# Kernel optimization log

Measured on AMD Instinct MI355X. Metric: run time of the kernel, lower is better.

## Reference

```python
import jax, jax.numpy as jnp
import numpy as np
from math import sqrt

N_HEADS = 4
IN_FEATURES = 64
KQ = 64
HEAD_V = IN_FEATURES // N_HEADS  # 16


def setup_inputs() -> dict:
    key = jax.random.key(0)
    ks = jax.random.split(key, 7)
    s = 0.05
    x = jax.random.normal(ks[0], (8192, IN_FEATURES), dtype=jnp.float32)
    # Per-head Linear weights stacked on a leading head axis.
    # torch Linear: y = x @ W.T + b; we store W already transposed: [H, F, E]
    Wq = jax.random.normal(ks[1], (N_HEADS, IN_FEATURES, KQ), dtype=jnp.float32) * s
    bq = jax.random.normal(ks[2], (N_HEADS, KQ), dtype=jnp.float32) * s
    Wk = jax.random.normal(ks[3], (N_HEADS, IN_FEATURES, KQ), dtype=jnp.float32) * s
    bk = jax.random.normal(ks[4], (N_HEADS, KQ), dtype=jnp.float32) * s
    Wv = jax.random.normal(ks[5], (N_HEADS, IN_FEATURES, HEAD_V), dtype=jnp.float32) * s
    bv = jax.random.normal(ks[6], (N_HEADS, HEAD_V), dtype=jnp.float32) * s
    return {"x": x, "Wq": Wq, "bq": bq, "Wk": Wk, "bk": bk, "Wv": Wv, "bv": bv}


def reference(x, Wq, bq, Wk, bk, Wv, bv):
    N, F = x.shape
    scale = 1.0 / sqrt(F)  # original divides by sqrt(in_features), NOT sqrt(kq)
    # Batched-head projections: [H, N, E]
    Q = jnp.einsum('nf,hfe->hne', x, Wq) + bq[:, None, :]
    K = jnp.einsum('nf,hfe->hne', x, Wk) + bk[:, None, :]
    V = jnp.einsum('nf,hfd->hnd', x, Wv) + bv[:, None, :]
    logits = jnp.einsum('hne,hme->hnm', Q, K) * scale  # [H, N, N]
    attn = jax.nn.softmax(logits, axis=-1)
    out_heads = jnp.einsum('hnm,hmd->hnd', attn, V)    # [H, N, HEAD_V]
    # Head i writes columns [i*HEAD_V:(i+1)*HEAD_V] of the output.
    out = jnp.transpose(out_heads, (1, 0, 2)).reshape(N, F)
    return out
```

## Files before the change

kernel.cpp:

```cpp
#include <hip/hip_runtime.h>

typedef __attribute__((ext_vector_type(4))) float f32x4;
typedef __attribute__((ext_vector_type(8))) short bf16x8;
typedef __attribute__((ext_vector_type(4))) short bf16x4;
typedef long fp8x8;

#define NH 4

static __device__ __forceinline__ unsigned short f2bf(float f){
  unsigned u = __float_as_uint(f);
  u += 0x7FFFu + ((u >> 16) & 1u);
  return (unsigned short)(u >> 16);
}

static __device__ __forceinline__ unsigned pack2bf(float a, float b){
  return __builtin_amdgcn_perm(__float_as_uint(b) + 0x8000u,
                               __float_as_uint(a) + 0x8000u, 0x07060302u);
}

static __device__ __forceinline__ int pack_fp8x4(float a, float b, float c, float d){
  int w = __builtin_amdgcn_cvt_pk_fp8_f32(a, b, 0, false);
  w     = __builtin_amdgcn_cvt_pk_fp8_f32(c, d, w, true);
  return w;
}

__global__ __launch_bounds__(256) void wprep_kernel(
    const float* __restrict__ Wq, const float* __restrict__ bq,
    const float* __restrict__ Wk, const float* __restrict__ bk,
    const float* __restrict__ Wv,
    unsigned short* __restrict__ WF, float* __restrict__ bias_s, int n)
{
  __shared__ unsigned short wqT[64*72];
  __shared__ unsigned short wkT[64*72];
  __shared__ unsigned short wvT[16*72];

  const int t = threadIdx.x;
  const int h = blockIdx.x;
  const float S1 = 0.4246609001f;
  const int f = t >> 2, eg = t & 3;

  {
    const float4* g = (const float4*)(Wq + h*4096 + f*64 + eg*16);
    #pragma unroll
    for (int p = 0; p < 4; ++p){
      float4 d = g[p];
      int e0 = eg*16 + p*4;
      wqT[(e0+0)*72 + f] = f2bf(d.x * S1);
      wqT[(e0+1)*72 + f] = f2bf(d.y * S1);
      wqT[(e0+2)*72 + f] = f2bf(d.z * S1);
      wqT[(e0+3)*72 + f] = f2bf(d.w * S1);
    }
  }
  {
    const float4* g = (const float4*)(Wk + h*4096 + f*64 + eg*16);
    #pragma unroll
    for (int p = 0; p < 4; ++p){
      float4 d = g[p];
      int e0 = eg*16 + p*4;
      wkT[(e0+0)*72 + f] = f2bf(d.x * S1);
      wkT[(e0+1)*72 + f] = f2bf(d.y * S1);
      wkT[(e0+2)*72 + f] = f2bf(d.z * S1);
      wkT[(e0+3)*72 + f] = f2bf(d.w * S1);
    }
  }
  {
    float4 d = *(const float4*)(Wv + h*1024 + f*16 + eg*4);
    int d0 = eg*4;
    wvT[(d0+0)*72 + f] = f2bf(d.x);
    wvT[(d0+1)*72 + f] = f2bf(d.y);
    wvT[(d0+2)*72 + f] = f2bf(d.z);
    wvT[(d0+3)*72 + f] = f2bf(d.w);
  }
  if (t < 64)       bias_s[h*128 + t] = bq[h*64 + t] * S1;
  else if (t < 128) bias_s[h*128 + t] = bk[h*64 + (t-64)] * S1;
  __syncthreads();

  const int lane = t & 63, w = t >> 6;
  const int quad = lane >> 4, l16 = lane & 15;
  for (int s = w; s < 18; s += 4){
    const unsigned short* src;
    if (s < 8){      int jt = s>>1,     ks = s&1;     src = wqT + (jt*16+l16)*72 + ks*32 + quad*8; }
    else if (s < 16){int ft = (s-8)>>1, ks = (s-8)&1; src = wkT + (ft*16+l16)*72 + ks*32 + quad*8; }
    else {           int ks = s-16;                   src = wvT + l16*72 + ks*32 + quad*8; }
    uint4 v = *(const uint4*)src;
    *(uint4*)(WF + ((size_t)(h*18 + s)*64 + lane)*8) = v;
  }
}

__global__ __launch_bounds__(256) void proj_kernel(
    const float* __restrict__ x, const float* __restrict__ bv,
    const unsigned short* __restrict__ WF, const float* __restrict__ bias_s,
    unsigned char* __restrict__ Qt, unsigned char* __restrict__ Kt,
    unsigned short* __restrict__ Vt, int n)
{
  __shared__ unsigned short xf[8*64*8];
  __shared__ float bql[64], bkl[64], bvl[16];

  const int t  = threadIdx.x;
  const int h  = blockIdx.y;
  const int r0 = blockIdx.x * 64;

  {
    const int r = t >> 2, cg4 = t & 3;
    const float4* g = (const float4*)(x + (size_t)(r0 + r)*64 + cg4*16);
    float4 a = g[0], b = g[1], c = g[2], d = g[3];
    unsigned u0 = pack2bf(a.x,a.y), u1 = pack2bf(a.z,a.w);
    unsigned u2 = pack2bf(b.x,b.y), u3 = pack2bf(b.z,b.w);
    unsigned u4 = pack2bf(c.x,c.y), u5 = pack2bf(c.z,c.w);
    unsigned u6 = pack2bf(d.x,d.y), u7 = pack2bf(d.z,d.w);
    const int it = r >> 4, l16r = r & 15, ks = cg4 >> 1, q0 = (cg4 & 1)*2;
    uint4* dst0 = (uint4*)(xf + ((it*2+ks)*64 + q0*16     + l16r)*8);
    uint4* dst1 = (uint4*)(xf + ((it*2+ks)*64 + (q0+1)*16 + l16r)*8);
    *dst0 = make_uint4(u0,u1,u2,u3);
    *dst1 = make_uint4(u4,u5,u6,u7);
  }
  if (t < 64)        bql[t]     = bias_s[h*128 + t];
  else if (t < 128)  bkl[t-64]  = bias_s[h*128 + t];
  else if (t < 144)  bvl[t-128] = bv[h*16 + (t-128)];
  __syncthreads();

  const int lane = t & 63, w = t >> 6;
  const int quad = lane >> 4, l16 = lane & 15;

  bf16x8 xa[8];
  #pragma unroll
  for (int i = 0; i < 8; ++i)
    xa[i] = *(const bf16x8*)(xf + (i*64 + lane)*8);

  const unsigned short* WFh = WF + (size_t)h*18*64*8;
  bf16x8 wq[8];
  #pragma unroll
  for (int s = 0; s < 8; ++s)
    wq[s] = *(const bf16x8*)(WFh + ((size_t)s*64 + lane)*8);
  bf16x8 wk0 = *(const bf16x8*)(WFh + ((size_t)(8 + w*2 + 0)*64 + lane)*8);
  bf16x8 wk1 = *(const bf16x8*)(WFh + ((size_t)(8 + w*2 + 1)*64 + lane)*8);
  bf16x8 wv0 = *(const bf16x8*)(WFh + ((size_t)16*64 + lane)*8);
  bf16x8 wv1 = *(const bf16x8*)(WFh + ((size_t)17*64 + lane)*8);

  const f32x4 z = {0.f,0.f,0.f,0.f};
  f32x4 accQ[4] = {z,z,z,z};
  f32x4 accK[4] = {z,z,z,z};
  f32x4 accV = z;

  #pragma unroll
  for (int jt = 0; jt < 4; ++jt){
    accQ[jt] = __builtin_amdgcn_mfma_f32_16x16x32_bf16(xa[w*2+0], wq[jt*2+0], accQ[jt], 0,0,0);
    accQ[jt] = __builtin_amdgcn_mfma_f32_16x16x32_bf16(xa[w*2+1], wq[jt*2+1], accQ[jt], 0,0,0);
  }
  #pragma unroll
  for (int tt = 0; tt < 4; ++tt){
    accK[tt] = __builtin_amdgcn_mfma_f32_16x16x32_bf16(wk0, xa[tt*2+0], accK[tt], 0,0,0);
    accK[tt] = __builtin_amdgcn_mfma_f32_16x16x32_bf16(wk1, xa[tt*2+1], accK[tt], 0,0,0);
  }
  accV = __builtin_amdgcn_mfma_f32_16x16x32_bf16(xa[w*2+0], wv0, accV, 0,0,0);
  accV = __builtin_amdgcn_mfma_f32_16x16x32_bf16(xa[w*2+1], wv1, accV, 0,0,0);

  #pragma unroll
  for (int jt = 0; jt < 4; ++jt){
    float bqv = bql[jt*16 + l16];
    unsigned o = pack_fp8x4(accQ[jt][0]+bqv, accQ[jt][1]+bqv,
                            accQ[jt][2]+bqv, accQ[jt][3]+bqv);
    *(unsigned*)(Qt + ((size_t)(h*64 + jt*16 + l16))*n + r0 + w*16 + quad*4) = o;
  }
  {
    const int f0 = w*16 + quad*4;
    const float bk0 = bkl[f0], bk1 = bkl[f0+1], bk2 = bkl[f0+2], bk3 = bkl[f0+3];
    const int qk = (f0 & 31) >> 3, hf = f0 >> 5, boff = (quad & 1) * 4;
    #pragma unroll
    for (int tt = 0; tt < 4; ++tt){
      unsigned o = pack_fp8x4(accK[tt][0]+bk0, accK[tt][1]+bk1,
                              accK[tt][2]+bk2, accK[tt][3]+bk3);
      const int T = (r0 >> 4) + tt;
      *(unsigned*)(Kt + (size_t)h*((size_t)n<<6) + (size_t)T*1024
                      + (qk*16 + l16)*16 + hf*8 + boff) = o;
    }
  }
  {
    float bvv = bvl[l16];
    unsigned v01 = pack2bf(accV[0]+bvv, accV[1]+bvv);
    unsigned v23 = pack2bf(accV[2]+bvv, accV[3]+bvv);
    const int T = (r0 >> 4) + w;
    *(uint2*)(Vt + (size_t)h*((size_t)n<<4) + ((size_t)T*64 + lane)*4) = make_uint2(v01, v23);
  }
}

__global__ __launch_bounds__(512) void attn_kernel(
    const unsigned char* __restrict__ Qt, const unsigned char* __restrict__ Kt,
    const unsigned short* __restrict__ Vt, float* __restrict__ out, int n)
{
  __shared__ float part[6][64][17];

  const int tid  = threadIdx.x;
  const int lane = tid & 63;
  const int w    = tid >> 6;
  const int rg   = w >> 2;
  const int jq   = w & 3;
  const int bid  = blockIdx.x;
  const int h    = bid & 3;
  const int iblk = bid >> 2;
  const int l16  = lane & 15, quad = lane >> 4;
  const int i0   = iblk*64 + rg*32;
  const int ntiles = (n >> 2) >> 4;
  const int tile0  = jq * ntiles;

  const unsigned char* qh = Qt + (size_t)(h*64)*n;
  fp8x8 qf[4];
  #pragma unroll
  for (int v = 0; v < 4; ++v){
    const int row0 = i0 + (v >> 1)*16;
    const int kb   = (v & 1)*32;
    const unsigned char* qp = qh + (size_t)(kb + quad*8)*n + row0 + l16;
    unsigned u0 = 0, u1 = 0;
    #pragma unroll
    for (int j = 0; j < 4; ++j) u0 |= (unsigned)qp[(size_t)j*n] << (8*j);
    #pragma unroll
    for (int j = 0; j < 4; ++j) u1 |= (unsigned)qp[(size_t)(j+4)*n] << (8*j);
    qf[v] = (fp8x8)(((unsigned long long)u1 << 32) | (unsigned long long)u0);
  }
  const fp8x8 qf00 = qf[0], qf01 = qf[1], qf10 = qf[2], qf11 = qf[3];

  const uint4* ktu = (const uint4*)(Kt + (size_t)h*((size_t)n<<6)) + (size_t)tile0*64 + lane;
  const uint2* vtu = (const uint2*)(Vt + (size_t)h*((size_t)n<<4)) + (size_t)tile0*64 + lane;

  f32x4 o0  = {0.f,0.f,0.f,0.f};
  f32x4 o1  = {0.f,0.f,0.f,0.f};
  f32x4 la0 = {0.f,0.f,0.f,0.f};
  f32x4 la1 = {0.f,0.f,0.f,0.f};
  const f32x4 z = {0.f,0.f,0.f,0.f};
  const bf16x4 vones = {(short)0x3F80, (short)0x3F80, (short)0x3F80, (short)0x3F80};

  uint4 ka = ktu[0];
  uint2 va = vtu[0];
  uint4 kb = ktu[64];
  uint2 vb = vtu[64];

  for (int tt = 0; tt < ntiles; tt += 2){
    int tn = tt + 2; if (tn >= ntiles) tn = 0;
    uint4 kc = ktu[(size_t)tn*64];
    uint2 vc = vtu[(size_t)tn*64];
    uint4 kd = ktu[(size_t)(tn+1)*64];
    uint2 vd = vtu[(size_t)(tn+1)*64];

    {
      fp8x8 k0 = (fp8x8)(((unsigned long long)ka.y << 32) | ka.x);
      fp8x8 k1 = (fp8x8)(((unsigned long long)ka.w << 32) | ka.z);
      bf16x4 vf; { union { uint2 u; bf16x4 v; } c; c.u = va; vf = c.v; }

      f32x4 s0 = __builtin_amdgcn_mfma_f32_16x16x32_fp8_fp8(k0, qf00, z, 0, 0, 0);
      s0 = __builtin_amdgcn_mfma_f32_16x16x32_fp8_fp8(k1, qf01, s0, 0, 0, 0);
      f32x4 s1 = __builtin_amdgcn_mfma_f32_16x16x32_fp8_fp8(k0, qf10, z, 0, 0, 0);
      s1 = __builtin_amdgcn_mfma_f32_16x16x32_fp8_fp8(k1, qf11, s1, 0, 0, 0);

      float p00 = __builtin_amdgcn_exp2f(s0[0]);
      float p01 = __builtin_amdgcn_exp2f(s0[1]);
      float p02 = __builtin_amdgcn_exp2f(s0[2]);
      float p03 = __builtin_amdgcn_exp2f(s0[3]);
      float p10 = __builtin_amdgcn_exp2f(s1[0]);
      float p11 = __builtin_amdgcn_exp2f(s1[1]);
      float p12 = __builtin_amdgcn_exp2f(s1[2]);
      float p13 = __builtin_amdgcn_exp2f(s1[3]);

      union { uint2 u; bf16x4 v; } pc0, pc1;
      pc0.u = make_uint2(pack2bf(p00,p01), pack2bf(p02,p03));
      pc1.u = make_uint2(pack2bf(p10,p11), pack2bf(p12,p13));
      o0  = __builtin_amdgcn_mfma_f32_16x16x16bf16_1k(pc0.v, vf,    o0,  0, 0, 0);
      o1  = __builtin_amdgcn_mfma_f32_16x16x16bf16_1k(pc1.v, vf,    o1,  0, 0, 0);
      la0 = __builtin_amdgcn_mfma_f32_16x16x16bf16_1k(pc0.v, vones, la0, 0, 0, 0);
      la1 = __builtin_amdgcn_mfma_f32_16x16x16bf16_1k(pc1.v, vones, la1, 0, 0, 0);
    }
    {
      fp8x8 k0 = (fp8x8)(((unsigned long long)kb.y << 32) | kb.x);
      fp8x8 k1 = (fp8x8)(((unsigned long long)kb.w << 32) | kb.z);
      bf16x4 vf; { union { uint2 u; bf16x4 v; } c; c.u = vb; vf = c.v; }

      f32x4 s0 = __builtin_amdgcn_mfma_f32_16x16x32_fp8_fp8(k0, qf00, z, 0, 0, 0);
      s0 = __builtin_amdgcn_mfma_f32_16x16x32_fp8_fp8(k1, qf01, s0, 0, 0, 0);
      f32x4 s1 = __builtin_amdgcn_mfma_f32_16x16x32_fp8_fp8(k0, qf10, z, 0, 0, 0);
      s1 = __builtin_amdgcn_mfma_f32_16x16x32_fp8_fp8(k1, qf11, s1, 0, 0, 0);

      float p00 = __builtin_amdgcn_exp2f(s0[0]);
      float p01 = __builtin_amdgcn_exp2f(s0[1]);
      float p02 = __builtin_amdgcn_exp2f(s0[2]);
      float p03 = __builtin_amdgcn_exp2f(s0[3]);
      float p10 = __builtin_amdgcn_exp2f(s1[0]);
      float p11 = __builtin_amdgcn_exp2f(s1[1]);
      float p12 = __builtin_amdgcn_exp2f(s1[2]);
      float p13 = __builtin_amdgcn_exp2f(s1[3]);

      union { uint2 u; bf16x4 v; } pc0, pc1;
      pc0.u = make_uint2(pack2bf(p00,p01), pack2bf(p02,p03));
      pc1.u = make_uint2(pack2bf(p10,p11), pack2bf(p12,p13));
      o0  = __builtin_amdgcn_mfma_f32_16x16x16bf16_1k(pc0.v, vf,    o0,  0, 0, 0);
      o1  = __builtin_amdgcn_mfma_f32_16x16x16bf16_1k(pc1.v, vf,    o1,  0, 0, 0);
      la0 = __builtin_amdgcn_mfma_f32_16x16x16bf16_1k(pc0.v, vones, la0, 0, 0, 0);
      la1 = __builtin_amdgcn_mfma_f32_16x16x16bf16_1k(pc1.v, vones, la1, 0, 0, 0);
    }

    ka = kc; va = vc;
    kb = kd; vb = vd;
  }

  if (jq > 0){
    float* p = &part[rg*3 + (jq-1)][lane][0];
    p[ 0]=o0[0];  p[ 1]=o0[1];  p[ 2]=o0[2];  p[ 3]=o0[3];
    p[ 4]=o1[0];  p[ 5]=o1[1];  p[ 6]=o1[2];  p[ 7]=o1[3];
    p[ 8]=la0[0]; p[ 9]=la0[1]; p[10]=la0[2]; p[11]=la0[3];
    p[12]=la1[0]; p[13]=la1[1]; p[14]=la1[2]; p[15]=la1[3];
  }
  __syncthreads();

  if (jq == 0){
    #pragma unroll
    for (int q = 0; q < 3; ++q){
      const float* r = &part[rg*3 + q][lane][0];
      o0[0] +=r[0];  o0[1] +=r[1];  o0[2] +=r[2];  o0[3] +=r[3];
      o1[0] +=r[4];  o1[1] +=r[5];  o1[2] +=r[6];  o1[3] +=r[7];
      la0[0]+=r[8];  la0[1]+=r[9];  la0[2]+=r[10]; la0[3]+=r[11];
      la1[0]+=r[12]; la1[1]+=r[13]; la1[2]+=r[14]; la1[3]+=r[15];
    }
    #pragma unroll
    for (int reg = 0; reg < 4; ++reg){
      int i = quad*4 + reg;
      out[(size_t)(i0 + i)*64      + h*16 + l16] = o0[reg] / la0[reg];
      out[(size_t)(i0 + 16 + i)*64 + h*16 + l16] = o1[reg] / la1[reg];
    }
  }
}

extern "C" void kernel_launch(void* const* d_in, const int* in_sizes, int n_in,
                              void* d_out, int out_size, void* d_ws, size_t ws_size,
                              hipStream_t stream) {
  const float* x  = (const float*)d_in[0];
  const float* Wq = (const float*)d_in[1];
  const float* bq = (const float*)d_in[2];
  const float* Wk = (const float*)d_in[3];
  const float* bk = (const float*)d_in[4];
  const float* Wv = (const float*)d_in[5];
  const float* bv = (const float*)d_in[6];
  float* out = (float*)d_out;

  const int n = in_sizes[0] / 64;

  unsigned char* Qt   = (unsigned char*)d_ws;
  unsigned char* Kt   = Qt + (size_t)NH*64*n;
  unsigned short* Vt  = (unsigned short*)(Kt + (size_t)NH*n*64);
  unsigned short* WF  = Vt + (size_t)NH*n*16;
  float* bias_s       = (float*)(WF + (size_t)NH*18*64*8);

  wprep_kernel<<<NH, 256, 0, stream>>>(Wq, bq, Wk, bk, Wv, WF, bias_s, n);
  proj_kernel<<<dim3(n/64, NH), 256, 0, stream>>>(x, bv, WF, bias_s, Qt, Kt, Vt, n);
  attn_kernel<<<dim3((n/64)*NH), 512, 0, stream>>>(Qt, Kt, Vt, out, n);
}
```

Measured before the change: 133.3 us.

## Store Q in MFMA fragment layout and split attention keys across eight waves

The projection kernel now writes Q in the same tiled fragment layout as K, so each attention wave loads its Q operands with two 16-byte vector loads instead of many strided byte loads. The attention kernel changes from two row groups of four key-splitting waves to one 32-row group whose eight waves each take an eighth of the keys, and the grid doubles in block count. This is meant to raise parallelism and cut per-block Q gather cost. In exchange, the LDS cross-wave reduction grows to seven partials, and each key and value tile is re-read by twice as many blocks.

```diff
diff --git a/kernel.cpp b/kernel.cpp
--- a/kernel.cpp
+++ b/kernel.cpp
@@ -79,7 +79,7 @@
   const int quad = lane >> 4, l16 = lane & 15;
   for (int s = w; s < 18; s += 4){
     const unsigned short* src;
-    if (s < 8){      int jt = s>>1,     ks = s&1;     src = wqT + (jt*16+l16)*72 + ks*32 + quad*8; }
+    if (s < 8){      int et = s>>1,     ks = s&1;     src = wqT + (et*16+l16)*72 + ks*32 + quad*8; }
     else if (s < 16){int ft = (s-8)>>1, ks = (s-8)&1; src = wkT + (ft*16+l16)*72 + ks*32 + quad*8; }
     else {           int ks = s-16;                   src = wvT + l16*72 + ks*32 + quad*8; }
     uint4 v = *(const uint4*)src;
@@ -90,7 +90,7 @@
 __global__ __launch_bounds__(256) void proj_kernel(
     const float* __restrict__ x, const float* __restrict__ bv,
     const unsigned short* __restrict__ WF, const float* __restrict__ bias_s,
-    unsigned char* __restrict__ Qt, unsigned char* __restrict__ Kt,
+    unsigned char* __restrict__ Qfr, unsigned char* __restrict__ Kt,
     unsigned short* __restrict__ Vt, int n)
 {
   __shared__ unsigned short xf[8*64*8];
@@ -128,12 +128,10 @@
     xa[i] = *(const bf16x8*)(xf + (i*64 + lane)*8);
 
   const unsigned short* WFh = WF + (size_t)h*18*64*8;
-  bf16x8 wq[8];
-  #pragma unroll
-  for (int s = 0; s < 8; ++s)
-    wq[s] = *(const bf16x8*)(WFh + ((size_t)s*64 + lane)*8);
-  bf16x8 wk0 = *(const bf16x8*)(WFh + ((size_t)(8 + w*2 + 0)*64 + lane)*8);
-  bf16x8 wk1 = *(const bf16x8*)(WFh + ((size_t)(8 + w*2 + 1)*64 + lane)*8);
+  bf16x8 wq0 = *(const bf16x8*)(WFh + ((size_t)(     w*2 + 0)*64 + lane)*8);
+  bf16x8 wq1 = *(const bf16x8*)(WFh + ((size_t)(     w*2 + 1)*64 + lane)*8);
+  bf16x8 wk0 = *(const bf16x8*)(WFh + ((size_t)(8  + w*2 + 0)*64 + lane)*8);
+  bf16x8 wk1 = *(const bf16x8*)(WFh + ((size_t)(8  + w*2 + 1)*64 + lane)*8);
   bf16x8 wv0 = *(const bf16x8*)(WFh + ((size_t)16*64 + lane)*8);
   bf16x8 wv1 = *(const bf16x8*)(WFh + ((size_t)17*64 + lane)*8);
 
@@ -143,9 +141,9 @@
   f32x4 accV = z;
 
   #pragma unroll
-  for (int jt = 0; jt < 4; ++jt){
-    accQ[jt] = __builtin_amdgcn_mfma_f32_16x16x32_bf16(xa[w*2+0], wq[jt*2+0], accQ[jt], 0,0,0);
-    accQ[jt] = __builtin_amdgcn_mfma_f32_16x16x32_bf16(xa[w*2+1], wq[jt*2+1], accQ[jt], 0,0,0);
+  for (int it = 0; it < 4; ++it){
+    accQ[it] = __builtin_amdgcn_mfma_f32_16x16x32_bf16(wq0, xa[it*2+0], accQ[it], 0,0,0);
+    accQ[it] = __builtin_amdgcn_mfma_f32_16x16x32_bf16(wq1, xa[it*2+1], accQ[it], 0,0,0);
   }
   #pragma unroll
   for (int tt = 0; tt < 4; ++tt){
@@ -155,12 +153,18 @@
   accV = __builtin_amdgcn_mfma_f32_16x16x32_bf16(xa[w*2+0], wv0, accV, 0,0,0);
   accV = __builtin_amdgcn_mfma_f32_16x16x32_bf16(xa[w*2+1], wv1, accV, 0,0,0);
 
-  #pragma unroll
-  for (int jt = 0; jt < 4; ++jt){
-    float bqv = bql[jt*16 + l16];
-    unsigned o = pack_fp8x4(accQ[jt][0]+bqv, accQ[jt][1]+bqv,
-                            accQ[jt][2]+bqv, accQ[jt][3]+bqv);
-    *(unsigned*)(Qt + ((size_t)(h*64 + jt*16 + l16))*n + r0 + w*16 + quad*4) = o;
+  {
+    const int e0 = w*16 + quad*4;
+    const float b0 = bql[e0], b1 = bql[e0+1], b2 = bql[e0+2], b3 = bql[e0+3];
+    const int qk = (e0 & 31) >> 3, hf = e0 >> 5, boff = (quad & 1) * 4;
+    #pragma unroll
+    for (int it = 0; it < 4; ++it){
+      unsigned o = pack_fp8x4(accQ[it][0]+b0, accQ[it][1]+b1,
+                              accQ[it][2]+b2, accQ[it][3]+b3);
+      const int T = (r0 >> 4) + it;
+      *(unsigned*)(Qfr + (size_t)h*((size_t)n<<6) + (size_t)T*1024
+                       + (qk*16 + l16)*16 + hf*8 + boff) = o;
+    }
   }
   {
     const int f0 = w*16 + quad*4;
@@ -185,39 +189,29 @@
 }
 
 __global__ __launch_bounds__(512) void attn_kernel(
-    const unsigned char* __restrict__ Qt, const unsigned char* __restrict__ Kt,
+    const unsigned char* __restrict__ Qfr, const unsigned char* __restrict__ Kt,
     const unsigned short* __restrict__ Vt, float* __restrict__ out, int n)
 {
-  __shared__ float part[6][64][17];
+  __shared__ float part[7][64][17];
 
   const int tid  = threadIdx.x;
   const int lane = tid & 63;
-  const int w    = tid >> 6;
-  const int rg   = w >> 2;
-  const int jq   = w & 3;
+  const int jq   = tid >> 6;
   const int bid  = blockIdx.x;
   const int h    = bid & 3;
   const int iblk = bid >> 2;
   const int l16  = lane & 15, quad = lane >> 4;
-  const int i0   = iblk*64 + rg*32;
-  const int ntiles = (n >> 2) >> 4;
-  const int tile0  = jq * ntiles;
-
-  const unsigned char* qh = Qt + (size_t)(h*64)*n;
-  fp8x8 qf[4];
-  #pragma unroll
-  for (int v = 0; v < 4; ++v){
-    const int row0 = i0 + (v >> 1)*16;
-    const int kb   = (v & 1)*32;
-    const unsigned char* qp = qh + (size_t)(kb + quad*8)*n + row0 + l16;
-    unsigned u0 = 0, u1 = 0;
-    #pragma unroll
-    for (int j = 0; j < 4; ++j) u0 |= (unsigned)qp[(size_t)j*n] << (8*j);
-    #pragma unroll
-    for (int j = 0; j < 4; ++j) u1 |= (unsigned)qp[(size_t)(j+4)*n] << (8*j);
-    qf[v] = (fp8x8)(((unsigned long long)u1 << 32) | (unsigned long long)u0);
-  }
-  const fp8x8 qf00 = qf[0], qf01 = qf[1], qf10 = qf[2], qf11 = qf[3];
+  const int i0   = iblk*32;
+  const int ntq  = (n >> 3) >> 4;
+  const int tile0 = jq * ntq;
+
+  const unsigned char* qfh = Qfr + (size_t)h*((size_t)n<<6);
+  uint4 q0 = *(const uint4*)(qfh + (size_t)((i0>>4)    )*1024 + lane*16);
+  uint4 q1 = *(const uint4*)(qfh + (size_t)((i0>>4) + 1)*1024 + lane*16);
+  const fp8x8 qf00 = (fp8x8)(((unsigned long long)q0.y << 32) | q0.x);
+  const fp8x8 qf01 = (fp8x8)(((unsigned long long)q0.w << 32) | q0.z);
+  const fp8x8 qf10 = (fp8x8)(((unsigned long long)q1.y << 32) | q1.x);
+  const fp8x8 qf11 = (fp8x8)(((unsigned long long)q1.w << 32) | q1.z);
 
   const uint4* ktu = (const uint4*)(Kt + (size_t)h*((size_t)n<<6)) + (size_t)tile0*64 + lane;
   const uint2* vtu = (const uint2*)(Vt + (size_t)h*((size_t)n<<4)) + (size_t)tile0*64 + lane;
@@ -234,8 +228,8 @@
   uint4 kb = ktu[64];
   uint2 vb = vtu[64];
 
-  for (int tt = 0; tt < ntiles; tt += 2){
-    int tn = tt + 2; if (tn >= ntiles) tn = 0;
+  for (int tt = 0; tt < ntq; tt += 2){
+    int tn = tt + 2; if (tn >= ntq) tn = 0;
     uint4 kc = ktu[(size_t)tn*64];
     uint2 vc = vtu[(size_t)tn*64];
     uint4 kd = ktu[(size_t)(tn+1)*64];
@@ -301,7 +295,7 @@
   }
 
   if (jq > 0){
-    float* p = &part[rg*3 + (jq-1)][lane][0];
+    float* p = &part[jq-1][lane][0];
     p[ 0]=o0[0];  p[ 1]=o0[1];  p[ 2]=o0[2];  p[ 3]=o0[3];
     p[ 4]=o1[0];  p[ 5]=o1[1];  p[ 6]=o1[2];  p[ 7]=o1[3];
     p[ 8]=la0[0]; p[ 9]=la0[1]; p[10]=la0[2]; p[11]=la0[3];
@@ -311,8 +305,8 @@
 
   if (jq == 0){
     #pragma unroll
-    for (int q = 0; q < 3; ++q){
-      const float* r = &part[rg*3 + q][lane][0];
+    for (int q = 0; q < 7; ++q){
+      const float* r = &part[q][lane][0];
       o0[0] +=r[0];  o0[1] +=r[1];  o0[2] +=r[2];  o0[3] +=r[3];
       o1[0] +=r[4];  o1[1] +=r[5];  o1[2] +=r[6];  o1[3] +=r[7];
       la0[0]+=r[8];  la0[1]+=r[9];  la0[2]+=r[10]; la0[3]+=r[11];
@@ -341,13 +335,13 @@
 
   const int n = in_sizes[0] / 64;
 
-  unsigned char* Qt   = (unsigned char*)d_ws;
-  unsigned char* Kt   = Qt + (size_t)NH*64*n;
+  unsigned char* Qfr  = (unsigned char*)d_ws;
+  unsigned char* Kt   = Qfr + (size_t)NH*n*64;
   unsigned short* Vt  = (unsigned short*)(Kt + (size_t)NH*n*64);
   unsigned short* WF  = Vt + (size_t)NH*n*16;
   float* bias_s       = (float*)(WF + (size_t)NH*18*64*8);
 
   wprep_kernel<<<NH, 256, 0, stream>>>(Wq, bq, Wk, bk, Wv, WF, bias_s, n);
-  proj_kernel<<<dim3(n/64, NH), 256, 0, stream>>>(x, bv, WF, bias_s, Qt, Kt, Vt, n);
-  attn_kernel<<<dim3((n/64)*NH), 512, 0, stream>>>(Qt, Kt, Vt, out, n);
-}
+  proj_kernel<<<dim3(n/64, NH), 256, 0, stream>>>(x, bv, WF, bias_s, Qfr, Kt, Vt, n);
+  attn_kernel<<<dim3((n/32)*NH), 512, 0, stream>>>(Qfr, Kt, Vt, out, n);
+}
```

Result: faster. 128.2 us (-3.8%).
